# Kernel optimization log

Measured on AMD Instinct MI355X. Metric: run time of the kernel, lower is better.

Reference implementation:

```python
import jax, jax.numpy as jnp
import numpy as np

HIDDEN = 128
NUM_BASIS = 50
NUM_FILTERS = 128
CUTOFF = 10.0
N_NODES = 20000
N_EDGES = 640000
LOG2 = 0.6931471805599453


def ssp(x):
    # ShiftedSoftplus: softplus(x) - log(2)
    return jax.nn.softplus(x) - LOG2


def setup_inputs() -> dict:
    key = jax.random.key(0)
    ks = jax.random.split(key, 10)
    def xavier(k, shape):
        fan_in, fan_out = shape[0], shape[1]
        a = jnp.sqrt(6.0 / (fan_in + fan_out))
        return jax.random.uniform(k, shape, jnp.float32, -a, a)
    x = jax.random.normal(ks[0], (N_NODES, HIDDEN), jnp.float32)
    edge_index = jax.random.randint(ks[1], (2, N_EDGES), 0, N_NODES, jnp.int64)
    edge_weight = jax.random.uniform(ks[2], (N_EDGES,), jnp.float32) * CUTOFF
    edge_attr = jax.random.normal(ks[3], (N_EDGES, NUM_BASIS), jnp.float32)
    return {
        "x": x,
        "edge_index": edge_index,
        "edge_weight": edge_weight,
        "edge_attr": edge_attr,
        "mlp_w1": xavier(ks[4], (NUM_BASIS, NUM_FILTERS)),
        "mlp_b1": jnp.zeros((NUM_FILTERS,), jnp.float32),
        "mlp_w2": xavier(ks[5], (NUM_FILTERS, NUM_FILTERS)),
        "mlp_b2": jnp.zeros((NUM_FILTERS,), jnp.float32),
        "lin1_w": xavier(ks[6], (HIDDEN, NUM_FILTERS)),
        "lin2_w": xavier(ks[7], (NUM_FILTERS, HIDDEN)),
        "lin2_b": jnp.zeros((HIDDEN,), jnp.float32),
        "lin_w": xavier(ks[8], (HIDDEN, HIDDEN)),
        "lin_b": jnp.zeros((HIDDEN,), jnp.float32),
    }


def reference(x, edge_index, edge_weight, edge_attr,
              mlp_w1, mlp_b1, mlp_w2, mlp_b2,
              lin1_w, lin2_w, lin2_b, lin_w, lin_b):
    src, dst = edge_index[0], edge_index[1]
    # cosine cutoff on edge distance  [E]
    C = 0.5 * (jnp.cos(edge_weight * (jnp.pi / CUTOFF)) + 1.0)
    # filter MLP on expanded basis  [E, F]
    W = ssp(edge_attr @ mlp_w1 + mlp_b1) @ mlp_w2 + mlp_b2
    W = W * C[:, None]
    # CFConv: gather source node features, weight, scatter-add to targets
    h = x @ lin1_w                      # [N, F]
    msg = h[src] * W                    # [E, F]
    agg = jax.ops.segment_sum(msg, dst, num_segments=N_NODES)  # [N, F]
    h = agg @ lin2_w + lin2_b           # [N, H]
    # interaction block tail
    h = ssp(h)
    out = h @ lin_w + lin_b             # [N, H]
    return out
```

## Files before the change

### kernel.cpp

```cpp
#include <hip/hip_runtime.h>
#include <hip/hip_bf16.h>

#define NNODES 20000
#define NEDGES 640000
#define NB 50
#define NF 128

typedef unsigned int uint_t;
typedef unsigned short ushort_t;

typedef __bf16 bf16x8 __attribute__((ext_vector_type(8)));
typedef float f32x4 __attribute__((ext_vector_type(4)));

__device__ __forceinline__ uint_t f2bf(float f) {
    uint_t u = __float_as_uint(f);
    return (u + 0x7fffu + ((u >> 16) & 1u)) >> 16;
}

__device__ __forceinline__ float ssp_f(float x) {
    float t = __expf(-fabsf(x));
    return fmaxf(x, 0.0f) + __logf(1.0f + t) - 0.6931471805599453f;
}

__global__ __launch_bounds__(256) void k_zero(float4* __restrict__ p) {
    int i = blockIdx.x * 256 + threadIdx.x;
    p[i] = make_float4(0.f, 0.f, 0.f, 0.f);
}

__global__ __launch_bounds__(256) void k_node1(const float* __restrict__ X,
                                               const float* __restrict__ W,
                                               float* __restrict__ Y, int nrows)
{
    __shared__ alignas(16) ushort_t sx[64 * 136];
    const int tid  = threadIdx.x;
    const int wv   = tid >> 6, lane = tid & 63;
    const int col  = lane & 15, quad = lane >> 4;

    bf16x8 wf[2][4];
    #pragma unroll
    for (int nt = 0; nt < 2; ++nt) {
        int n = wv * 32 + nt * 16 + col;
        #pragma unroll
        for (int kc = 0; kc < 4; ++kc)
            #pragma unroll
            for (int j = 0; j < 8; ++j)
                wf[nt][kc][j] = (__bf16)W[(kc * 32 + quad * 8 + j) * NF + n];
    }

    const int rbase = blockIdx.x * 64;
    for (int i = tid; i < 64 * 64; i += 256) {
        int r = i >> 6, c = i & 63;
        int gr = rbase + r;
        float2 v = (gr < nrows) ? *reinterpret_cast<const float2*>(&X[(size_t)gr * NF + 2 * c])
                                : make_float2(0.f, 0.f);
        reinterpret_cast<uint_t*>(sx)[r * 68 + c] = f2bf(v.x) | (f2bf(v.y) << 16);
    }
    __syncthreads();

    f32x4 acc[4][2] = {};
    #pragma unroll
    for (int kc = 0; kc < 4; ++kc) {
        bf16x8 af[4];
        #pragma unroll
        for (int mt = 0; mt < 4; ++mt)
            af[mt] = *reinterpret_cast<const bf16x8*>(&sx[(mt * 16 + col) * 136 + kc * 32 + quad * 8]);
        #pragma unroll
        for (int mt = 0; mt < 4; ++mt)
            #pragma unroll
            for (int nt = 0; nt < 2; ++nt)
                acc[mt][nt] = __builtin_amdgcn_mfma_f32_16x16x32_bf16(af[mt], wf[nt][kc], acc[mt][nt], 0, 0, 0);
    }
    #pragma unroll
    for (int mt = 0; mt < 4; ++mt)
        #pragma unroll
        for (int nt = 0; nt < 2; ++nt)
            #pragma unroll
            for (int r = 0; r < 4; ++r) {
                int row = rbase + mt * 16 + quad * 4 + r;
                if (row < nrows) Y[(size_t)row * NF + wv * 32 + nt * 16 + col] = acc[mt][nt][r];
            }
}

__global__ __launch_bounds__(256) void k_tail(const float* __restrict__ X,
                                              const float* __restrict__ W1, const float* __restrict__ B1,
                                              const float* __restrict__ W2, const float* __restrict__ B2,
                                              float* __restrict__ Y, int nrows)
{
    __shared__ alignas(16) ushort_t sx[64 * 136];
    __shared__ alignas(16) ushort_t st[64 * 136];
    const int tid  = threadIdx.x;
    const int wv   = tid >> 6, lane = tid & 63;
    const int col  = lane & 15, quad = lane >> 4;

    bf16x8 wf1[2][4], wf2[2][4];
    float rb1[2], rb2[2];
    #pragma unroll
    for (int nt = 0; nt < 2; ++nt) {
        int n = wv * 32 + nt * 16 + col;
        rb1[nt] = B1[n]; rb2[nt] = B2[n];
        #pragma unroll
        for (int kc = 0; kc < 4; ++kc)
            #pragma unroll
            for (int j = 0; j < 8; ++j) {
                int k = kc * 32 + quad * 8 + j;
                wf1[nt][kc][j] = (__bf16)W1[k * NF + n];
                wf2[nt][kc][j] = (__bf16)W2[k * NF + n];
            }
    }

    const int rbase = blockIdx.x * 64;
    for (int i = tid; i < 64 * 64; i += 256) {
        int r = i >> 6, c = i & 63;
        int gr = rbase + r;
        float2 v = (gr < nrows) ? *reinterpret_cast<const float2*>(&X[(size_t)gr * NF + 2 * c])
                                : make_float2(0.f, 0.f);
        reinterpret_cast<uint_t*>(sx)[r * 68 + c] = f2bf(v.x) | (f2bf(v.y) << 16);
    }
    __syncthreads();

    f32x4 acc[4][2];
    #pragma unroll
    for (int mt = 0; mt < 4; ++mt)
        #pragma unroll
        for (int nt = 0; nt < 2; ++nt)
            acc[mt][nt] = f32x4{rb1[nt], rb1[nt], rb1[nt], rb1[nt]};
    #pragma unroll
    for (int kc = 0; kc < 4; ++kc) {
        bf16x8 af[4];
        #pragma unroll
        for (int mt = 0; mt < 4; ++mt)
            af[mt] = *reinterpret_cast<const bf16x8*>(&sx[(mt * 16 + col) * 136 + kc * 32 + quad * 8]);
        #pragma unroll
        for (int mt = 0; mt < 4; ++mt)
            #pragma unroll
            for (int nt = 0; nt < 2; ++nt)
                acc[mt][nt] = __builtin_amdgcn_mfma_f32_16x16x32_bf16(af[mt], wf1[nt][kc], acc[mt][nt], 0, 0, 0);
    }
    #pragma unroll
    for (int mt = 0; mt < 4; ++mt)
        #pragma unroll
        for (int nt = 0; nt < 2; ++nt)
            #pragma unroll
            for (int r = 0; r < 4; ++r)
                st[(mt * 16 + quad * 4 + r) * 136 + wv * 32 + nt * 16 + col] =
                    (ushort_t)f2bf(ssp_f(acc[mt][nt][r]));
    __syncthreads();

    f32x4 acc2[4][2];
    #pragma unroll
    for (int mt = 0; mt < 4; ++mt)
        #pragma unroll
        for (int nt = 0; nt < 2; ++nt)
            acc2[mt][nt] = f32x4{rb2[nt], rb2[nt], rb2[nt], rb2[nt]};
    #pragma unroll
    for (int kc = 0; kc < 4; ++kc) {
        bf16x8 af[4];
        #pragma unroll
        for (int mt = 0; mt < 4; ++mt)
            af[mt] = *reinterpret_cast<const bf16x8*>(&st[(mt * 16 + col) * 136 + kc * 32 + quad * 8]);
        #pragma unroll
        for (int mt = 0; mt < 4; ++mt)
            #pragma unroll
            for (int nt = 0; nt < 2; ++nt)
                acc2[mt][nt] = __builtin_amdgcn_mfma_f32_16x16x32_bf16(af[mt], wf2[nt][kc], acc2[mt][nt], 0, 0, 0);
    }
    #pragma unroll
    for (int mt = 0; mt < 4; ++mt)
        #pragma unroll
        for (int nt = 0; nt < 2; ++nt)
            #pragma unroll
            for (int r = 0; r < 4; ++r) {
                int row = rbase + mt * 16 + quad * 4 + r;
                if (row < nrows) Y[(size_t)row * NF + wv * 32 + nt * 16 + col] = acc2[mt][nt][r];
            }
}

__global__ __launch_bounds__(256) void k_edge(
    const int* __restrict__ esrc, const int* __restrict__ edst,
    const float* __restrict__ ew, const float* __restrict__ ea,
    const float* __restrict__ w1, const float* __restrict__ b1,
    const float* __restrict__ w2, const float* __restrict__ b2,
    const float* __restrict__ h, float* __restrict__ agg)
{
    __shared__ alignas(16) ushort_t w1f[16 * 64 * 8];
    __shared__ alignas(16) ushort_t w2f[32 * 64 * 8];
    __shared__ alignas(16) ushort_t st1[4][16 * 72];

    const int tid  = threadIdx.x;
    const int wv   = tid >> 6, lane = tid & 63;
    const int col  = lane & 15, quad = lane >> 4;

    for (int idx = tid; idx < 16 * 64; idx += 256) {
        int fr = idx >> 6, l = idx & 63;
        int ntg = fr >> 1, kc = fr & 1;
        int n = ntg * 16 + (l & 15), kb = kc * 32 + (l >> 4) * 8;
        ushort_t* d = &w1f[idx * 8];
        #pragma unroll
        for (int j = 0; j < 8; ++j) {
            int k = kb + j;
            d[j] = (ushort_t)((k < NB) ? f2bf(w1[k * NF + n]) : 0u);
        }
    }
    for (int idx = tid; idx < 32 * 64; idx += 256) {
        int fr = idx >> 6, l = idx & 63;
        int ntg = fr >> 2, kc = fr & 3;
        int n = ntg * 16 + (l & 15), kb = kc * 32 + (l >> 4) * 8;
        ushort_t* d = &w2f[idx * 8];
        #pragma unroll
        for (int j = 0; j < 8; ++j)
            d[j] = (ushort_t)f2bf(w2[(kb + j) * NF + n]);
    }
    float rb1[8], rb2[8];
    #pragma unroll
    for (int nt = 0; nt < 8; ++nt) { rb1[nt] = b1[nt * 16 + col]; rb2[nt] = b2[nt * 16 + col]; }
    __syncthreads();

    ushort_t* myst = st1[wv];

    for (int it = 0; it < 5; ++it) {
        const int ebase = blockIdx.x * 320 + wv * 80 + it * 16;

        int srcv[4], dstv[4];
        float Cw[4];
        #pragma unroll
        for (int r = 0; r < 4; ++r) {
            int e = ebase + quad * 4 + r;
            srcv[r] = esrc[e];
            dstv[r] = edst[e];
            Cw[r]   = 0.5f * (__cosf(ew[e] * 0.31415926535897931f) + 1.0f);
        }

        float hg[8][4];
        #pragma unroll
        for (int nt = 0; nt < 8; ++nt)
            #pragma unroll
            for (int r = 0; r < 4; ++r)
                hg[nt][r] = h[(size_t)srcv[r] * NF + nt * 16 + col];

        const float* erow = ea + (size_t)(ebase + col) * NB;
        bf16x8 af0, af1;
        #pragma unroll
        for (int p = 0; p < 4; ++p) {
            float2 v = *reinterpret_cast<const float2*>(erow + quad * 8 + 2 * p);
            af0[2 * p]     = (__bf16)v.x;
            af0[2 * p + 1] = (__bf16)v.y;
        }
        #pragma unroll
        for (int p = 0; p < 4; ++p) {
            int k = 32 + quad * 8 + 2 * p;
            float2 v = (k + 2 <= NB) ? *reinterpret_cast<const float2*>(erow + k)
                                     : make_float2(0.f, 0.f);
            af1[2 * p]     = (__bf16)v.x;
            af1[2 * p + 1] = (__bf16)v.y;
        }

        f32x4 acc2[8];
        #pragma unroll
        for (int nt = 0; nt < 8; ++nt) acc2[nt] = f32x4{rb2[nt], rb2[nt], rb2[nt], rb2[nt]};

        #pragma unroll
        for (int hf = 0; hf < 2; ++hf) {
            f32x4 acc1[4];
            #pragma unroll
            for (int nt = 0; nt < 4; ++nt) {
                int ntg = hf * 4 + nt;
                acc1[nt] = f32x4{rb1[ntg], rb1[ntg], rb1[ntg], rb1[ntg]};
                bf16x8 bw0 = *reinterpret_cast<const bf16x8*>(&w1f[((ntg * 2 + 0) * 64 + lane) * 8]);
                bf16x8 bw1 = *reinterpret_cast<const bf16x8*>(&w1f[((ntg * 2 + 1) * 64 + lane) * 8]);
                acc1[nt] = __builtin_amdgcn_mfma_f32_16x16x32_bf16(af0, bw0, acc1[nt], 0, 0, 0);
                acc1[nt] = __builtin_amdgcn_mfma_f32_16x16x32_bf16(af1, bw1, acc1[nt], 0, 0, 0);
            }
            #pragma unroll
            for (int nt = 0; nt < 4; ++nt)
                #pragma unroll
                for (int r = 0; r < 4; ++r)
                    myst[(quad * 4 + r) * 72 + nt * 16 + col] = (ushort_t)f2bf(ssp_f(acc1[nt][r]));
            bf16x8 a20 = *reinterpret_cast<const bf16x8*>(&myst[col * 72 + 0 * 32 + quad * 8]);
            bf16x8 a21 = *reinterpret_cast<const bf16x8*>(&myst[col * 72 + 1 * 32 + quad * 8]);
            #pragma unroll
            for (int nt = 0; nt < 8; ++nt) {
                bf16x8 b20 = *reinterpret_cast<const bf16x8*>(&w2f[((nt * 4 + hf * 2 + 0) * 64 + lane) * 8]);
                bf16x8 b21 = *reinterpret_cast<const bf16x8*>(&w2f[((nt * 4 + hf * 2 + 1) * 64 + lane) * 8]);
                acc2[nt] = __builtin_amdgcn_mfma_f32_16x16x32_bf16(a20, b20, acc2[nt], 0, 0, 0);
                acc2[nt] = __builtin_amdgcn_mfma_f32_16x16x32_bf16(a21, b21, acc2[nt], 0, 0, 0);
            }
        }

        #pragma unroll
        for (int nt = 0; nt < 8; ++nt)
            #pragma unroll
            for (int r = 0; r < 4; ++r)
                atomicAdd(&agg[(size_t)dstv[r] * NF + nt * 16 + col],
                          acc2[nt][r] * Cw[r] * hg[nt][r]);
    }
}

extern "C" void kernel_launch(void* const* d_in, const int* in_sizes, int n_in,
                              void* d_out, int out_size, void* d_ws, size_t ws_size,
                              hipStream_t stream) {
    const float* x    = (const float*)d_in[0];
    const int*   eidx = (const int*)d_in[1];
    const float* ew   = (const float*)d_in[2];
    const float* ea   = (const float*)d_in[3];
    const float* w1   = (const float*)d_in[4];
    const float* b1   = (const float*)d_in[5];
    const float* w2   = (const float*)d_in[6];
    const float* b2   = (const float*)d_in[7];
    const float* l1w  = (const float*)d_in[8];
    const float* l2w  = (const float*)d_in[9];
    const float* l2b  = (const float*)d_in[10];
    const float* lw   = (const float*)d_in[11];
    const float* lb   = (const float*)d_in[12];
    (void)in_sizes; (void)n_in; (void)out_size; (void)ws_size;

    float* h   = (float*)d_ws;
    float* agg = (float*)((char*)d_ws + (size_t)NNODES * NF * 4);

    hipLaunchKernelGGL(k_zero, dim3(2500), dim3(256), 0, stream, (float4*)agg);
    hipLaunchKernelGGL(k_node1, dim3(313), dim3(256), 0, stream, x, l1w, h, NNODES);
    hipLaunchKernelGGL(k_edge, dim3(2000), dim3(256), 0, stream,
                       eidx, eidx + NEDGES, ew, ea, w1, b1, w2, b2, h, agg);
    hipLaunchKernelGGL(k_tail, dim3(313), dim3(256), 0, stream,
                       agg, l2w, l2b, lw, lb, (float*)d_out, NNODES);
}
```

Measured before the change: 591.9 us.

## Replace atomic scatter-add with CSR sort by destination and gather aggregation

Builds a destination-sorted CSR (histogram, scan, scatter permutation) each call. The edge kernel writes per-edge messages as bf16 to a buffer, and a per-node kernel gathers and sums them, which removes the float atomics on agg. This adds about 164MB of message write plus read traffic, several extra launches and a single-block scan. It also rounds messages to bf16 before summation. The old atomic path is kept as a fallback when the workspace is too small.

```diff
diff --git a/kernel.cpp b/kernel.cpp
--- a/kernel.cpp
+++ b/kernel.cpp
@@ -12,6 +12,9 @@
 typedef __bf16 bf16x8 __attribute__((ext_vector_type(8)));
 typedef float f32x4 __attribute__((ext_vector_type(4)));
 
+__device__ __forceinline__ float lo16(uint_t u) { return __uint_as_float(u << 16); }
+__device__ __forceinline__ float hi16(uint_t u) { return __uint_as_float(u & 0xffff0000u); }
+
 __device__ __forceinline__ uint_t f2bf(float f) {
     uint_t u = __float_as_uint(f);
     return (u + 0x7fffu + ((u >> 16) & 1u)) >> 16;
@@ -25,6 +28,71 @@
 __global__ __launch_bounds__(256) void k_zero(float4* __restrict__ p) {
     int i = blockIdx.x * 256 + threadIdx.x;
     p[i] = make_float4(0.f, 0.f, 0.f, 0.f);
+}
+
+__global__ __launch_bounds__(256) void k_zero_small(int* __restrict__ p, int n) {
+    int i = blockIdx.x * 256 + threadIdx.x;
+    if (i < n) p[i] = 0;
+}
+
+__global__ __launch_bounds__(256) void k_hist(const int* __restrict__ dst, int* __restrict__ hist) {
+    int i = blockIdx.x * 256 + threadIdx.x;
+    if (i < NEDGES) atomicAdd(&hist[dst[i]], 1);
+}
+
+__global__ __launch_bounds__(1024) void k_scan(const int* __restrict__ hist, int* __restrict__ off) {
+    __shared__ int buf[1024];
+    __shared__ int carry;
+    if (threadIdx.x == 0) carry = 0;
+    __syncthreads();
+    for (int base = 0; base < NNODES; base += 1024) {
+        int i = base + (int)threadIdx.x;
+        int v = (i < NNODES) ? hist[i] : 0;
+        buf[threadIdx.x] = v;
+        __syncthreads();
+        for (int s = 1; s < 1024; s <<= 1) {
+            int t = (threadIdx.x >= (unsigned)s) ? buf[threadIdx.x - s] : 0;
+            __syncthreads();
+            buf[threadIdx.x] += t;
+            __syncthreads();
+        }
+        if (i < NNODES) off[i] = carry + buf[threadIdx.x] - v;
+        __syncthreads();
+        if (threadIdx.x == 1023) carry += buf[1023];
+        __syncthreads();
+    }
+    if (threadIdx.x == 0) off[NNODES] = NEDGES;
+}
+
+__global__ __launch_bounds__(256) void k_scatter(const int* __restrict__ dst,
+                                                 const int* __restrict__ off,
+                                                 int* __restrict__ cnt,
+                                                 int* __restrict__ perm) {
+    int i = blockIdx.x * 256 + threadIdx.x;
+    if (i < NEDGES) {
+        int d = dst[i];
+        int pos = off[d] + atomicAdd(&cnt[d], 1);
+        perm[pos] = i;
+    }
+}
+
+__global__ __launch_bounds__(256) void k_agg(const int* __restrict__ off,
+                                             const int* __restrict__ perm,
+                                             const ushort_t* __restrict__ msg,
+                                             float* __restrict__ agg) {
+    int node = blockIdx.x * 4 + (threadIdx.x >> 6);
+    int lane = threadIdx.x & 63;
+    if (node >= NNODES) return;
+    int s = off[node], e = off[node + 1];
+    float a0 = 0.f, a1 = 0.f;
+    #pragma unroll 4
+    for (int p = s; p < e; ++p) {
+        uint_t u = reinterpret_cast<const uint_t*>(msg)[(size_t)perm[p] * 64 + lane];
+        a0 += lo16(u);
+        a1 += hi16(u);
+    }
+    agg[(size_t)node * NF + 2 * lane]     = a0;
+    agg[(size_t)node * NF + 2 * lane + 1] = a1;
 }
 
 __global__ __launch_bounds__(256) void k_node1(const float* __restrict__ X,
@@ -175,12 +243,14 @@
             }
 }
 
+template<bool ATOMIC>
 __global__ __launch_bounds__(256) void k_edge(
     const int* __restrict__ esrc, const int* __restrict__ edst,
     const float* __restrict__ ew, const float* __restrict__ ea,
     const float* __restrict__ w1, const float* __restrict__ b1,
     const float* __restrict__ w2, const float* __restrict__ b2,
-    const float* __restrict__ h, float* __restrict__ agg)
+    const float* __restrict__ h, float* __restrict__ agg,
+    __bf16* __restrict__ msg)
 {
     __shared__ alignas(16) ushort_t w1f[16 * 64 * 8];
     __shared__ alignas(16) ushort_t w2f[32 * 64 * 8];
@@ -226,7 +296,7 @@
         for (int r = 0; r < 4; ++r) {
             int e = ebase + quad * 4 + r;
             srcv[r] = esrc[e];
-            dstv[r] = edst[e];
+            if (ATOMIC) dstv[r] = edst[e];
             Cw[r]   = 0.5f * (__cosf(ew[e] * 0.31415926535897931f) + 1.0f);
         }
 
@@ -289,9 +359,14 @@
         #pragma unroll
         for (int nt = 0; nt < 8; ++nt)
             #pragma unroll
-            for (int r = 0; r < 4; ++r)
-                atomicAdd(&agg[(size_t)dstv[r] * NF + nt * 16 + col],
-                          acc2[nt][r] * Cw[r] * hg[nt][r]);
+            for (int r = 0; r < 4; ++r) {
+                float v = acc2[nt][r] * Cw[r] * hg[nt][r];
+                if (ATOMIC) {
+                    atomicAdd(&agg[(size_t)dstv[r] * NF + nt * 16 + col], v);
+                } else {
+                    msg[(size_t)(ebase + quad * 4 + r) * NF + nt * 16 + col] = (__bf16)v;
+                }
+            }
     }
 }
 
@@ -311,15 +386,39 @@
     const float* l2b  = (const float*)d_in[10];
     const float* lw   = (const float*)d_in[11];
     const float* lb   = (const float*)d_in[12];
-    (void)in_sizes; (void)n_in; (void)out_size; (void)ws_size;
-
-    float* h   = (float*)d_ws;
-    float* agg = (float*)((char*)d_ws + (size_t)NNODES * NF * 4);
-
-    hipLaunchKernelGGL(k_zero, dim3(2500), dim3(256), 0, stream, (float4*)agg);
+    (void)in_sizes; (void)n_in; (void)out_size;
+
+    const int* esrc = eidx;
+    const int* edst = eidx + NEDGES;
+
+    char* p = (char*)d_ws;
+    float* h    = (float*)p;                 p += (size_t)NNODES * NF * 4;
+    float* agg  = (float*)p;                 p += (size_t)NNODES * NF * 4;
+    int*   off  = (int*)p;                   p += (size_t)(NNODES + 4) * 4;
+    int*   hist = (int*)p;                   p += (size_t)NNODES * 4;
+    int*   cnt  = (int*)p;                   p += (size_t)NNODES * 4;
+    int*   perm = (int*)p;                   p += (size_t)NEDGES * 4;
+    p = (char*)(((uintptr_t)p + 15) & ~(uintptr_t)15);
+    __bf16* msg = (__bf16*)p;                p += (size_t)NEDGES * NF * 2;
+    const bool two_phase = ((size_t)(p - (char*)d_ws) <= ws_size);
+
     hipLaunchKernelGGL(k_node1, dim3(313), dim3(256), 0, stream, x, l1w, h, NNODES);
-    hipLaunchKernelGGL(k_edge, dim3(2000), dim3(256), 0, stream,
-                       eidx, eidx + NEDGES, ew, ea, w1, b1, w2, b2, h, agg);
+
+    if (two_phase) {
+        hipLaunchKernelGGL(k_zero_small, dim3(157), dim3(256), 0, stream, hist, 2 * NNODES);
+        hipLaunchKernelGGL(k_hist, dim3(2500), dim3(256), 0, stream, edst, hist);
+        hipLaunchKernelGGL(k_scan, dim3(1), dim3(1024), 0, stream, hist, off);
+        hipLaunchKernelGGL(k_scatter, dim3(2500), dim3(256), 0, stream, edst, off, cnt, perm);
+        hipLaunchKernelGGL((k_edge<false>), dim3(2000), dim3(256), 0, stream,
+                           esrc, edst, ew, ea, w1, b1, w2, b2, h, agg, msg);
+        hipLaunchKernelGGL(k_agg, dim3(5000), dim3(256), 0, stream,
+                           off, perm, (const ushort_t*)msg, agg);
+    } else {
+        hipLaunchKernelGGL(k_zero, dim3(2500), dim3(256), 0, stream, (float4*)agg);
+        hipLaunchKernelGGL((k_edge<true>), dim3(2000), dim3(256), 0, stream,
+                           esrc, edst, ew, ea, w1, b1, w2, b2, h, agg, msg);
+    }
+
     hipLaunchKernelGGL(k_tail, dim3(313), dim3(256), 0, stream,
                        agg, l2w, l2b, lw, lb, (float*)d_out, NNODES);
 }
```

New measurement: 645.9 us. +9.1%, slower.

## Sort edges into destination CSR and accumulate per node instead of atomics

Applied to the files above, without the earlier changes.

Adds a preprocessing pipeline (histogram, block scan, offsets, scatter) that builds a destination-sorted CSR with a permutation, sorted source indices and precomputed cosine cutoffs. The edge kernel then walks one destination node per wave iteration, accumulates its messages in registers and writes agg once per node. This removes the float atomic scatter-add into agg and the separate zeroing kernel. In exchange it adds several small launches, an index permutation for the edge_attr gather, and wasted MFMA work on partial 16-edge tiles for nodes whose degree is not a multiple of 16. The manual bf16 rounding helper is also replaced with native __bf16 casts.

```diff
diff --git a/kernel.cpp b/kernel.cpp
--- a/kernel.cpp
+++ b/kernel.cpp
@@ -5,33 +5,85 @@
 #define NEDGES 640000
 #define NB 50
 #define NF 128
+#define NBLK_SCAN 79
 
 typedef unsigned int uint_t;
 typedef unsigned short ushort_t;
 
 typedef __bf16 bf16x8 __attribute__((ext_vector_type(8)));
 typedef float f32x4 __attribute__((ext_vector_type(4)));
-
-__device__ __forceinline__ uint_t f2bf(float f) {
-    uint_t u = __float_as_uint(f);
-    return (u + 0x7fffu + ((u >> 16) & 1u)) >> 16;
-}
 
 __device__ __forceinline__ float ssp_f(float x) {
     float t = __expf(-fabsf(x));
     return fmaxf(x, 0.0f) + __logf(1.0f + t) - 0.6931471805599453f;
 }
 
-__global__ __launch_bounds__(256) void k_zero(float4* __restrict__ p) {
+__global__ __launch_bounds__(256) void k_zero_small(int* __restrict__ p, int n) {
     int i = blockIdx.x * 256 + threadIdx.x;
-    p[i] = make_float4(0.f, 0.f, 0.f, 0.f);
+    if (i < n) p[i] = 0;
+}
+
+__global__ __launch_bounds__(256) void k_hist(const int* __restrict__ dst, int* __restrict__ hist) {
+    int i = blockIdx.x * 256 + threadIdx.x;
+    if (i < NEDGES) atomicAdd(&hist[dst[i]], 1);
+}
+
+__global__ __launch_bounds__(256) void k_bsum(const int* __restrict__ hist, int* __restrict__ bsum) {
+    __shared__ int ws[4];
+    int i = blockIdx.x * 256 + threadIdx.x;
+    int v = (i < NNODES) ? hist[i] : 0;
+    #pragma unroll
+    for (int s = 1; s < 64; s <<= 1) v += __shfl_xor(v, s, 64);
+    if ((threadIdx.x & 63) == 0) ws[threadIdx.x >> 6] = v;
+    __syncthreads();
+    if (threadIdx.x == 0) bsum[blockIdx.x] = ws[0] + ws[1] + ws[2] + ws[3];
+}
+
+__global__ __launch_bounds__(64) void k_scan_b(const int* __restrict__ bsum, int* __restrict__ bbase) {
+    if (threadIdx.x == 0) {
+        int acc = 0;
+        for (int b = 0; b < NBLK_SCAN; ++b) { bbase[b] = acc; acc += bsum[b]; }
+    }
+}
+
+__global__ __launch_bounds__(256) void k_off(const int* __restrict__ hist, const int* __restrict__ bbase,
+                                             int* __restrict__ off) {
+    __shared__ int buf[256];
+    int i = blockIdx.x * 256 + threadIdx.x;
+    int v = (i < NNODES) ? hist[i] : 0;
+    buf[threadIdx.x] = v;
+    __syncthreads();
+    #pragma unroll
+    for (int s = 1; s < 256; s <<= 1) {
+        int t = (threadIdx.x >= (unsigned)s) ? buf[threadIdx.x - s] : 0;
+        __syncthreads();
+        buf[threadIdx.x] += t;
+        __syncthreads();
+    }
+    if (i < NNODES) off[i] = bbase[blockIdx.x] + buf[threadIdx.x] - v;
+    if (i == NNODES) off[NNODES] = NEDGES;
+}
+
+__global__ __launch_bounds__(256) void k_scatter(const int* __restrict__ src, const int* __restrict__ dst,
+                                                 const float* __restrict__ ew,
+                                                 const int* __restrict__ off, int* __restrict__ cnt,
+                                                 int* __restrict__ perm, int* __restrict__ srcs,
+                                                 float* __restrict__ Cs) {
+    int i = blockIdx.x * 256 + threadIdx.x;
+    if (i < NEDGES) {
+        int d = dst[i];
+        int pos = off[d] + atomicAdd(&cnt[d], 1);
+        perm[pos] = i;
+        srcs[pos] = src[i];
+        Cs[pos]   = 0.5f * (__cosf(ew[i] * 0.31415926535897931f) + 1.0f);
+    }
 }
 
 __global__ __launch_bounds__(256) void k_node1(const float* __restrict__ X,
                                                const float* __restrict__ W,
                                                float* __restrict__ Y, int nrows)
 {
-    __shared__ alignas(16) ushort_t sx[64 * 136];
+    __shared__ alignas(16) __bf16 sx[64 * 136];
     const int tid  = threadIdx.x;
     const int wv   = tid >> 6, lane = tid & 63;
     const int col  = lane & 15, quad = lane >> 4;
@@ -53,7 +105,8 @@
         int gr = rbase + r;
         float2 v = (gr < nrows) ? *reinterpret_cast<const float2*>(&X[(size_t)gr * NF + 2 * c])
                                 : make_float2(0.f, 0.f);
-        reinterpret_cast<uint_t*>(sx)[r * 68 + c] = f2bf(v.x) | (f2bf(v.y) << 16);
+        sx[r * 136 + 2 * c]     = (__bf16)v.x;
+        sx[r * 136 + 2 * c + 1] = (__bf16)v.y;
     }
     __syncthreads();
 
@@ -86,8 +139,8 @@
                                               const float* __restrict__ W2, const float* __restrict__ B2,
                                               float* __restrict__ Y, int nrows)
 {
-    __shared__ alignas(16) ushort_t sx[64 * 136];
-    __shared__ alignas(16) ushort_t st[64 * 136];
+    __shared__ alignas(16) __bf16 sx[64 * 136];
+    __shared__ alignas(16) __bf16 st[64 * 136];
     const int tid  = threadIdx.x;
     const int wv   = tid >> 6, lane = tid & 63;
     const int col  = lane & 15, quad = lane >> 4;
@@ -114,7 +167,8 @@
         int gr = rbase + r;
         float2 v = (gr < nrows) ? *reinterpret_cast<const float2*>(&X[(size_t)gr * NF + 2 * c])
                                 : make_float2(0.f, 0.f);
-        reinterpret_cast<uint_t*>(sx)[r * 68 + c] = f2bf(v.x) | (f2bf(v.y) << 16);
+        sx[r * 136 + 2 * c]     = (__bf16)v.x;
+        sx[r * 136 + 2 * c + 1] = (__bf16)v.y;
     }
     __syncthreads();
 
@@ -142,8 +196,7 @@
         for (int nt = 0; nt < 2; ++nt)
             #pragma unroll
             for (int r = 0; r < 4; ++r)
-                st[(mt * 16 + quad * 4 + r) * 136 + wv * 32 + nt * 16 + col] =
-                    (ushort_t)f2bf(ssp_f(acc[mt][nt][r]));
+                st[(mt * 16 + quad * 4 + r) * 136 + wv * 32 + nt * 16 + col] = (__bf16)ssp_f(acc[mt][nt][r]);
     __syncthreads();
 
     f32x4 acc2[4][2];
@@ -175,16 +228,17 @@
             }
 }
 
-__global__ __launch_bounds__(256) void k_edge(
-    const int* __restrict__ esrc, const int* __restrict__ edst,
-    const float* __restrict__ ew, const float* __restrict__ ea,
+__global__ __launch_bounds__(256) void k_edge_csr(
+    const int* __restrict__ off, const int* __restrict__ perm,
+    const int* __restrict__ srcs, const float* __restrict__ Cs,
+    const float* __restrict__ ea,
     const float* __restrict__ w1, const float* __restrict__ b1,
     const float* __restrict__ w2, const float* __restrict__ b2,
     const float* __restrict__ h, float* __restrict__ agg)
 {
-    __shared__ alignas(16) ushort_t w1f[16 * 64 * 8];
-    __shared__ alignas(16) ushort_t w2f[32 * 64 * 8];
-    __shared__ alignas(16) ushort_t st1[4][16 * 72];
+    __shared__ alignas(16) __bf16 w1f[16 * 64 * 8];
+    __shared__ alignas(16) __bf16 w2f[32 * 64 * 8];
+    __shared__ alignas(16) __bf16 st1[4][16 * 72];
 
     const int tid  = threadIdx.x;
     const int wv   = tid >> 6, lane = tid & 63;
@@ -194,104 +248,124 @@
         int fr = idx >> 6, l = idx & 63;
         int ntg = fr >> 1, kc = fr & 1;
         int n = ntg * 16 + (l & 15), kb = kc * 32 + (l >> 4) * 8;
-        ushort_t* d = &w1f[idx * 8];
+        __bf16* d = &w1f[idx * 8];
         #pragma unroll
         for (int j = 0; j < 8; ++j) {
             int k = kb + j;
-            d[j] = (ushort_t)((k < NB) ? f2bf(w1[k * NF + n]) : 0u);
+            d[j] = (__bf16)((k < NB) ? w1[k * NF + n] : 0.0f);
         }
     }
     for (int idx = tid; idx < 32 * 64; idx += 256) {
         int fr = idx >> 6, l = idx & 63;
         int ntg = fr >> 2, kc = fr & 3;
         int n = ntg * 16 + (l & 15), kb = kc * 32 + (l >> 4) * 8;
-        ushort_t* d = &w2f[idx * 8];
+        __bf16* d = &w2f[idx * 8];
         #pragma unroll
         for (int j = 0; j < 8; ++j)
-            d[j] = (ushort_t)f2bf(w2[(kb + j) * NF + n]);
+            d[j] = (__bf16)w2[(kb + j) * NF + n];
     }
     float rb1[8], rb2[8];
     #pragma unroll
     for (int nt = 0; nt < 8; ++nt) { rb1[nt] = b1[nt * 16 + col]; rb2[nt] = b2[nt * 16 + col]; }
     __syncthreads();
 
-    ushort_t* myst = st1[wv];
-
-    for (int it = 0; it < 5; ++it) {
-        const int ebase = blockIdx.x * 320 + wv * 80 + it * 16;
-
-        int srcv[4], dstv[4];
-        float Cw[4];
-        #pragma unroll
-        for (int r = 0; r < 4; ++r) {
-            int e = ebase + quad * 4 + r;
-            srcv[r] = esrc[e];
-            dstv[r] = edst[e];
-            Cw[r]   = 0.5f * (__cosf(ew[e] * 0.31415926535897931f) + 1.0f);
-        }
-
-        float hg[8][4];
-        #pragma unroll
-        for (int nt = 0; nt < 8; ++nt)
-            #pragma unroll
-            for (int r = 0; r < 4; ++r)
-                hg[nt][r] = h[(size_t)srcv[r] * NF + nt * 16 + col];
-
-        const float* erow = ea + (size_t)(ebase + col) * NB;
-        bf16x8 af0, af1;
-        #pragma unroll
-        for (int p = 0; p < 4; ++p) {
-            float2 v = *reinterpret_cast<const float2*>(erow + quad * 8 + 2 * p);
-            af0[2 * p]     = (__bf16)v.x;
-            af0[2 * p + 1] = (__bf16)v.y;
-        }
-        #pragma unroll
-        for (int p = 0; p < 4; ++p) {
-            int k = 32 + quad * 8 + 2 * p;
-            float2 v = (k + 2 <= NB) ? *reinterpret_cast<const float2*>(erow + k)
-                                     : make_float2(0.f, 0.f);
-            af1[2 * p]     = (__bf16)v.x;
-            af1[2 * p + 1] = (__bf16)v.y;
-        }
-
-        f32x4 acc2[8];
-        #pragma unroll
-        for (int nt = 0; nt < 8; ++nt) acc2[nt] = f32x4{rb2[nt], rb2[nt], rb2[nt], rb2[nt]};
-
-        #pragma unroll
-        for (int hf = 0; hf < 2; ++hf) {
-            f32x4 acc1[4];
-            #pragma unroll
-            for (int nt = 0; nt < 4; ++nt) {
-                int ntg = hf * 4 + nt;
-                acc1[nt] = f32x4{rb1[ntg], rb1[ntg], rb1[ntg], rb1[ntg]};
-                bf16x8 bw0 = *reinterpret_cast<const bf16x8*>(&w1f[((ntg * 2 + 0) * 64 + lane) * 8]);
-                bf16x8 bw1 = *reinterpret_cast<const bf16x8*>(&w1f[((ntg * 2 + 1) * 64 + lane) * 8]);
-                acc1[nt] = __builtin_amdgcn_mfma_f32_16x16x32_bf16(af0, bw0, acc1[nt], 0, 0, 0);
-                acc1[nt] = __builtin_amdgcn_mfma_f32_16x16x32_bf16(af1, bw1, acc1[nt], 0, 0, 0);
-            }
-            #pragma unroll
-            for (int nt = 0; nt < 4; ++nt)
+    __bf16* myst = st1[wv];
+    const int gw = blockIdx.x * 4 + wv;
+
+    for (int ni = 0; ni < 5; ++ni) {
+        const int n = gw * 5 + ni;
+        const int s = off[n], eend = off[n + 1];
+
+        float pacc[8] = {0.f, 0.f, 0.f, 0.f, 0.f, 0.f, 0.f, 0.f};
+
+        for (int base = s; base < eend; base += 16) {
+            int pos  = base + col;
+            int lpos = min(pos, NEDGES - 1);
+            int eidc = perm[lpos];
+            int srcc = srcs[lpos];
+            float Cv = (pos < eend) ? Cs[lpos] : 0.0f;
+
+            int   src_r[4];
+            float Cw[4];
+            #pragma unroll
+            for (int r = 0; r < 4; ++r) {
+                int sl = quad * 4 + r;
+                src_r[r] = __shfl(srcc, sl, 64);
+                Cw[r]    = __shfl(Cv,   sl, 64);
+            }
+
+            float hg[8][4];
+            #pragma unroll
+            for (int nt = 0; nt < 8; ++nt)
                 #pragma unroll
                 for (int r = 0; r < 4; ++r)
-                    myst[(quad * 4 + r) * 72 + nt * 16 + col] = (ushort_t)f2bf(ssp_f(acc1[nt][r]));
-            bf16x8 a20 = *reinterpret_cast<const bf16x8*>(&myst[col * 72 + 0 * 32 + quad * 8]);
-            bf16x8 a21 = *reinterpret_cast<const bf16x8*>(&myst[col * 72 + 1 * 32 + quad * 8]);
-            #pragma unroll
-            for (int nt = 0; nt < 8; ++nt) {
-                bf16x8 b20 = *reinterpret_cast<const bf16x8*>(&w2f[((nt * 4 + hf * 2 + 0) * 64 + lane) * 8]);
-                bf16x8 b21 = *reinterpret_cast<const bf16x8*>(&w2f[((nt * 4 + hf * 2 + 1) * 64 + lane) * 8]);
-                acc2[nt] = __builtin_amdgcn_mfma_f32_16x16x32_bf16(a20, b20, acc2[nt], 0, 0, 0);
-                acc2[nt] = __builtin_amdgcn_mfma_f32_16x16x32_bf16(a21, b21, acc2[nt], 0, 0, 0);
-            }
+                    hg[nt][r] = h[(size_t)src_r[r] * NF + nt * 16 + col];
+
+            const float* erow = ea + (size_t)eidc * NB;
+            bf16x8 af0, af1;
+            #pragma unroll
+            for (int p = 0; p < 4; ++p) {
+                float2 v = *reinterpret_cast<const float2*>(erow + quad * 8 + 2 * p);
+                af0[2 * p]     = (__bf16)v.x;
+                af0[2 * p + 1] = (__bf16)v.y;
+            }
+            #pragma unroll
+            for (int p = 0; p < 4; ++p) {
+                int k = 32 + quad * 8 + 2 * p;
+                float2 v = (k + 2 <= NB) ? *reinterpret_cast<const float2*>(erow + k)
+                                         : make_float2(0.f, 0.f);
+                af1[2 * p]     = (__bf16)v.x;
+                af1[2 * p + 1] = (__bf16)v.y;
+            }
+
+            f32x4 acc2[8];
+            #pragma unroll
+            for (int nt = 0; nt < 8; ++nt) acc2[nt] = f32x4{rb2[nt], rb2[nt], rb2[nt], rb2[nt]};
+
+            #pragma unroll
+            for (int hf = 0; hf < 2; ++hf) {
+                f32x4 acc1[4];
+                #pragma unroll
+                for (int nt = 0; nt < 4; ++nt) {
+                    int ntg = hf * 4 + nt;
+                    acc1[nt] = f32x4{rb1[ntg], rb1[ntg], rb1[ntg], rb1[ntg]};
+                    bf16x8 bw0 = *reinterpret_cast<const bf16x8*>(&w1f[((ntg * 2 + 0) * 64 + lane) * 8]);
+                    bf16x8 bw1 = *reinterpret_cast<const bf16x8*>(&w1f[((ntg * 2 + 1) * 64 + lane) * 8]);
+                    acc1[nt] = __builtin_amdgcn_mfma_f32_16x16x32_bf16(af0, bw0, acc1[nt], 0, 0, 0);
+                    acc1[nt] = __builtin_amdgcn_mfma_f32_16x16x32_bf16(af1, bw1, acc1[nt], 0, 0, 0);
+                }
+                #pragma unroll
+                for (int nt = 0; nt < 4; ++nt)
+                    #pragma unroll
+                    for (int r = 0; r < 4; ++r)
+                        myst[(quad * 4 + r) * 72 + nt * 16 + col] = (__bf16)ssp_f(acc1[nt][r]);
+                bf16x8 a20 = *reinterpret_cast<const bf16x8*>(&myst[col * 72 + 0 * 32 + quad * 8]);
+                bf16x8 a21 = *reinterpret_cast<const bf16x8*>(&myst[col * 72 + 1 * 32 + quad * 8]);
+                #pragma unroll
+                for (int nt = 0; nt < 8; ++nt) {
+                    bf16x8 b20 = *reinterpret_cast<const bf16x8*>(&w2f[((nt * 4 + hf * 2 + 0) * 64 + lane) * 8]);
+                    bf16x8 b21 = *reinterpret_cast<const bf16x8*>(&w2f[((nt * 4 + hf * 2 + 1) * 64 + lane) * 8]);
+                    acc2[nt] = __builtin_amdgcn_mfma_f32_16x16x32_bf16(a20, b20, acc2[nt], 0, 0, 0);
+                    acc2[nt] = __builtin_amdgcn_mfma_f32_16x16x32_bf16(a21, b21, acc2[nt], 0, 0, 0);
+                }
+            }
+
+            #pragma unroll
+            for (int nt = 0; nt < 8; ++nt)
+                #pragma unroll
+                for (int r = 0; r < 4; ++r) {
+                    float t = Cw[r] * hg[nt][r];
+                    pacc[nt] = fmaf(acc2[nt][r], t, pacc[nt]);
+                }
         }
 
         #pragma unroll
-        for (int nt = 0; nt < 8; ++nt)
-            #pragma unroll
-            for (int r = 0; r < 4; ++r)
-                atomicAdd(&agg[(size_t)dstv[r] * NF + nt * 16 + col],
-                          acc2[nt][r] * Cw[r] * hg[nt][r]);
+        for (int nt = 0; nt < 8; ++nt) {
+            float v = pacc[nt];
+            v += __shfl_xor(v, 16, 64);
+            v += __shfl_xor(v, 32, 64);
+            if (lane < 16) agg[(size_t)n * NF + nt * 16 + lane] = v;
+        }
     }
 }
 
@@ -313,13 +387,34 @@
     const float* lb   = (const float*)d_in[12];
     (void)in_sizes; (void)n_in; (void)out_size; (void)ws_size;
 
-    float* h   = (float*)d_ws;
-    float* agg = (float*)((char*)d_ws + (size_t)NNODES * NF * 4);
-
-    hipLaunchKernelGGL(k_zero, dim3(2500), dim3(256), 0, stream, (float4*)agg);
+    const int* esrc = eidx;
+    const int* edst = eidx + NEDGES;
+
+    char* p = (char*)d_ws;
+    float* h    = (float*)p;  p += (size_t)NNODES * NF * 4;
+    float* agg  = (float*)p;  p += (size_t)NNODES * NF * 4;
+    int*   off  = (int*)p;    p += (size_t)(NNODES + 4) * 4;
+    int*   hist = (int*)p;    p += (size_t)NNODES * 4;
+    int*   cnt  = (int*)p;    p += (size_t)NNODES * 4;
+    int*   bsum = (int*)p;    p += 128 * 4;
+    int*   bbase= (int*)p;    p += 128 * 4;
+    int*   perm = (int*)p;    p += (size_t)NEDGES * 4;
+    int*   srcs = (int*)p;    p += (size_t)NEDGES * 4;
+    float* Cs   = (float*)p;  p += (size_t)NEDGES * 4;
+
     hipLaunchKernelGGL(k_node1, dim3(313), dim3(256), 0, stream, x, l1w, h, NNODES);
-    hipLaunchKernelGGL(k_edge, dim3(2000), dim3(256), 0, stream,
-                       eidx, eidx + NEDGES, ew, ea, w1, b1, w2, b2, h, agg);
+
+    hipLaunchKernelGGL(k_zero_small, dim3(157), dim3(256), 0, stream, hist, 2 * NNODES);
+    hipLaunchKernelGGL(k_hist, dim3(2500), dim3(256), 0, stream, edst, hist);
+    hipLaunchKernelGGL(k_bsum, dim3(NBLK_SCAN), dim3(256), 0, stream, hist, bsum);
+    hipLaunchKernelGGL(k_scan_b, dim3(1), dim3(64), 0, stream, bsum, bbase);
+    hipLaunchKernelGGL(k_off, dim3(NBLK_SCAN), dim3(256), 0, stream, hist, bbase, off);
+    hipLaunchKernelGGL(k_scatter, dim3(2500), dim3(256), 0, stream,
+                       esrc, edst, ew, off, cnt, perm, srcs, Cs);
+
+    hipLaunchKernelGGL(k_edge_csr, dim3(1000), dim3(256), 0, stream,
+                       off, perm, srcs, Cs, ea, w1, b1, w2, b2, h, agg);
+
     hipLaunchKernelGGL(k_tail, dim3(313), dim3(256), 0, stream,
                        agg, l2w, l2b, lw, lb, (float*)d_out, NNODES);
 }
```

After: 559.0 us. 1.06x faster.
